# Kernel optimization log

Hardware: AMD Instinct MI355X
Metric: run time of the kernel (lower is better)

Reference implementation:

```python
import jax, jax.numpy as jnp
import numpy as np

T = 262144
S_IN, A_IN, S_OUT, G_OUT, H = 64, 16, 32, 16, 32


def setup_inputs() -> dict:
    key = jax.random.key(0)
    ks = jax.random.split(key, 16)
    def lin_w(k, i, o):
        return (jax.random.normal(k, (i, o), jnp.float32) / np.sqrt(i)).astype(jnp.float32)
    return {
        's': jax.random.normal(ks[0], (1, T, S_IN), jnp.float32),
        'a': jax.random.uniform(ks[1], (1, T, A_IN), jnp.float32),  # BCE targets in [0,1]
        'u': jax.random.uniform(ks[2], (1, T, 1), jnp.float32),     # Bernoulli noise
        'W1': lin_w(ks[3], 2 * (S_IN + A_IN), H), 'b1': jnp.zeros((H,), jnp.float32),
        'W2': lin_w(ks[4], 2 * H, H),             'b2': jnp.zeros((H,), jnp.float32),
        'W3': lin_w(ks[5], 2 * H, S_OUT + G_OUT + 1), 'b3': jnp.zeros((S_OUT + G_OUT + 1,), jnp.float32),
        'Wp1': lin_w(ks[6], S_IN + G_OUT, H),     'bp1': jnp.zeros((H,), jnp.float32),
        'Wp2': lin_w(ks[7], H, A_IN),             'bp2': jnp.zeros((A_IN,), jnp.float32),
    }


def gnn_layer(x, W, b):
    # GraphNetLayer: each node sees its own feature + global mean over the trajectory
    agg = jnp.broadcast_to(jnp.mean(x, axis=1, keepdims=True), x.shape)
    return jnp.concatenate([x, agg], axis=-1) @ W + b


def reference(s, a, u, W1, b1, W2, b2, W3, b3, Wp1, bp1, Wp2, bp2):
    # encode: GNN over [N,T,s_in+a_in]
    x = jnp.concatenate([s, a], axis=-1)
    h = jnp.tanh(gnn_layer(x, W1, b1))
    h = jnp.tanh(gnn_layer(h, W2, b2))
    out = gnn_layer(h, W3, b3)
    z, g, alpha_logit = jnp.split(out, [S_OUT, S_OUT + G_OUT], axis=-1)
    alpha = jax.nn.sigmoid(alpha_logit)

    # Bernoulli sample with externalized noise; no gradient through the sample
    hard_alpha = jax.lax.stop_gradient((u < alpha).astype(alpha.dtype))  # [1,T,1]
    log_probs = hard_alpha * jax.nn.log_sigmoid(alpha_logit) + (1.0 - hard_alpha) * jax.nn.log_sigmoid(-alpha_logit)
    reinforce_lp = jnp.mean(log_probs)

    # extend_goals_hard: carry last goal where alpha fired (N==1), ragged scan
    def step(prev, ga):
        gt, at = ga  # [G_OUT], [1]
        cur = jnp.where(at > 0, gt, prev)
        return cur, cur
    _, hard_g = jax.lax.scan(step, jnp.zeros((G_OUT,), g.dtype), (g[0], hard_alpha[0]))
    hard_g = hard_g[None]  # [1,T,G_OUT]

    # decode: goal-conditioned policy MLP
    logits = jnp.tanh(jnp.concatenate([s, hard_g], axis=-1) @ Wp1 + bp1) @ Wp2 + bp2

    # BCEWithLogits recon loss (use_prior=False, train_dynamics/correspondence=False)
    recon = -(a * jax.nn.log_sigmoid(logits) + (1.0 - a) * jax.nn.log_sigmoid(-logits))
    per_ts = recon
    loss = jnp.mean(per_ts) + reinforce_lp * jnp.mean(jax.lax.stop_gradient(per_ts))

    # padded equivalents of short_z/short_g (ragged gather z[0,mask]) returned as masked tensors
    return loss, logits, hard_alpha, hard_g
```

## Files before the change

kernel.cpp:

```cpp
#include <hip/hip_runtime.h>
#include <math.h>


#define TT 262144
#define NBT 1024
#define NBR 512

__device__ __forceinline__ float spf32(float x) {
  return fmaxf(x, 0.f) + log1pf(expf(-fabsf(x)));
}

__device__ __forceinline__ double exp64(double x) {
  const double LOG2E  = 1.4426950408889634074;
  const double LN2_HI = 6.93147180369123816490e-01;
  const double LN2_LO = 1.90821492927058770002e-10;
  double kd = rint(x * LOG2E);
  double r  = fma(-kd, LN2_HI, x);
  r = fma(-kd, LN2_LO, r);
  double p = 2.08767569878681e-9;
  p = fma(p, r, 2.505210838544172e-8);
  p = fma(p, r, 2.755731922398589e-7);
  p = fma(p, r, 2.7557319223985893e-6);
  p = fma(p, r, 2.48015873015873e-5);
  p = fma(p, r, 1.984126984126984e-4);
  p = fma(p, r, 1.388888888888889e-3);
  p = fma(p, r, 8.333333333333333e-3);
  p = fma(p, r, 4.1666666666666664e-2);
  p = fma(p, r, 1.6666666666666666e-1);
  p = fma(p, r, 0.5);
  p = fma(p, r, 1.0);
  p = fma(p, r, 1.0);
  int k = (int)kd;
  long long sb = ((long long)(k + 1023)) << 52;
  return p * __longlong_as_double(sb);
}

__device__ __forceinline__ double tanh64(double x) {
  double ax = fmin(fabs(x), 19.0);
  double e = exp64(2.0 * ax);
  double t = 1.0 - 2.0 / (e + 1.0);
  return x >= 0.0 ? t : -t;
}

template <int C>
__global__ __launch_bounds__(256) void reduce_cols(const float* __restrict__ in,
                                                   double* __restrict__ part) {
  const int rpb = 256 / C;
  int col = threadIdx.x & (C - 1);
  int sub = threadIdx.x / C;
  long row0 = (long)blockIdx.x * rpb + sub;
  long stride = (long)NBR * rpb;
  double acc = 0.0;
  for (long r = row0; r < TT; r += stride) acc += (double)in[r * C + col];
  __shared__ double sm[256];
  sm[threadIdx.x] = acc;
  __syncthreads();
  if (threadIdx.x < C) {
    double s = 0.0;
#pragma unroll
    for (int i = 0; i < rpb; ++i) s += sm[i * C + threadIdx.x];
    part[(long)blockIdx.x * C + threadIdx.x] = s;
  }
}

__global__ __launch_bounds__(640) void prep1(const double* __restrict__ ps_s,
                                             const double* __restrict__ ps_a,
                                             const float* __restrict__ W1,
                                             const float* __restrict__ b1,
                                             double invT, double* __restrict__ c1) {
  __shared__ double partial[80][8];
  __shared__ double mx[80];
  int tid = threadIdx.x;
  int col = tid >> 3, sub = tid & 7;
  double ssum = 0.0;
  if (col < 64) {
#pragma unroll
    for (int i = 0; i < 64; ++i) ssum += ps_s[(sub * 64 + i) * 64 + col];
  } else {
    int c = col - 64;
#pragma unroll
    for (int i = 0; i < 64; ++i) ssum += ps_a[(sub * 64 + i) * 16 + c];
  }
  partial[col][sub] = ssum;
  __syncthreads();
  if (tid < 80) {
    double s = 0.0;
#pragma unroll
    for (int i = 0; i < 8; ++i) s += partial[tid][i];
    mx[tid] = s * invT;
  }
  __syncthreads();
  if (tid < 32) {
    double acc = (double)b1[tid];
    for (int j = 0; j < 80; ++j) acc += mx[j] * (double)W1[(80 + j) * 32 + tid];
    c1[tid] = acc;
  }
}

__global__ __launch_bounds__(256) void prep2(const double* __restrict__ ps,
                                             const float* __restrict__ W2,
                                             const float* __restrict__ b2,
                                             double invT, double* __restrict__ c2) {
  __shared__ double partial[32][8];
  __shared__ double mh[32];
  int tid = threadIdx.x;
  int col = tid >> 3, sub = tid & 7;
  double ssum = 0.0;
#pragma unroll
  for (int i = 0; i < 128; ++i) ssum += ps[(sub * 128 + i) * 32 + col];
  partial[col][sub] = ssum;
  __syncthreads();
  if (tid < 32) {
    double s = 0.0;
#pragma unroll
    for (int i = 0; i < 8; ++i) s += partial[tid][i];
    mh[tid] = s * invT;
  }
  __syncthreads();
  if (tid < 32) {
    double acc = (double)b2[tid];
    for (int j = 0; j < 32; ++j) acc += mh[j] * (double)W2[(32 + j) * 32 + tid];
    c2[tid] = acc;
  }
}

__global__ __launch_bounds__(256) void prep3(const double* __restrict__ ps,
                                             const float* __restrict__ W3,
                                             const float* __restrict__ b3,
                                             double invT, double* __restrict__ c3) {
  __shared__ double partial[32][8];
  __shared__ double mh[32];
  int tid = threadIdx.x;
  int col = tid >> 3, sub = tid & 7;
  double ssum = 0.0;
#pragma unroll
  for (int i = 0; i < 128; ++i) ssum += ps[(sub * 128 + i) * 32 + col];
  partial[col][sub] = ssum;
  __syncthreads();
  if (tid < 32) {
    double s = 0.0;
#pragma unroll
    for (int i = 0; i < 8; ++i) s += partial[tid][i];
    mh[tid] = s * invT;
  }
  __syncthreads();
  if (tid < 17) {
    double acc = (double)b3[32 + tid];
    for (int j = 0; j < 32; ++j) acc += mh[j] * (double)W3[(32 + j) * 49 + 32 + tid];
    c3[tid] = acc;
  }
}


__global__ __launch_bounds__(256, 2) void h1_kernel(const float* __restrict__ s,
                                                    const float* __restrict__ a,
                                                    const float* __restrict__ W1,
                                                    const double* __restrict__ c1,
                                                    double* __restrict__ h,
                                                    double* __restrict__ ps_h) {
  __shared__ double Wl[80 * 32];
  __shared__ double ws[4 * 32];
  for (int i = threadIdx.x; i < 80 * 32; i += 256) Wl[i] = (double)W1[i];
  __syncthreads();
  long t = (long)blockIdx.x * 256 + threadIdx.x;
  double acc[32];
#pragma unroll
  for (int k = 0; k < 32; ++k) acc[k] = c1[k];
  const float4* s4 = (const float4*)(s + t * 64);
#pragma unroll 2
  for (int q = 0; q < 16; ++q) {
    float4 v = s4[q];
    const double* w = &Wl[(q * 4) * 32];
    double x0 = (double)v.x, x1 = (double)v.y, x2 = (double)v.z, x3 = (double)v.w;
#pragma unroll
    for (int k = 0; k < 32; ++k)
      acc[k] += x0 * w[k] + x1 * w[32 + k] + x2 * w[64 + k] + x3 * w[96 + k];
  }
  const float4* a4 = (const float4*)(a + t * 16);
#pragma unroll 2
  for (int q = 0; q < 4; ++q) {
    float4 v = a4[q];
    const double* w = &Wl[(64 + q * 4) * 32];
    double x0 = (double)v.x, x1 = (double)v.y, x2 = (double)v.z, x3 = (double)v.w;
#pragma unroll
    for (int k = 0; k < 32; ++k)
      acc[k] += x0 * w[k] + x1 * w[32 + k] + x2 * w[64 + k] + x3 * w[96 + k];
  }
  double* o = h + (size_t)blockIdx.x * 8192 + threadIdx.x;
#pragma unroll
  for (int k = 0; k < 32; ++k) { acc[k] = tanh64(acc[k]); o[k * 256] = acc[k]; }
  int lane = threadIdx.x & 63, wave = threadIdx.x >> 6;
#pragma unroll
  for (int k = 0; k < 32; ++k) {
    double v = acc[k];
    v += __shfl_down(v, 32, 64); v += __shfl_down(v, 16, 64);
    v += __shfl_down(v, 8, 64);  v += __shfl_down(v, 4, 64);
    v += __shfl_down(v, 2, 64);  v += __shfl_down(v, 1, 64);
    if (lane == 0) ws[wave * 32 + k] = v;
  }
  __syncthreads();
  if (threadIdx.x < 32) {
    double ssum = ws[threadIdx.x] + ws[32 + threadIdx.x] + ws[64 + threadIdx.x] +
                  ws[96 + threadIdx.x];
    ps_h[blockIdx.x * 32 + threadIdx.x] = ssum;
  }
}

__global__ __launch_bounds__(256, 2) void h2_kernel(const double* __restrict__ hin,
                                                    const float* __restrict__ W2,
                                                    const double* __restrict__ c2,
                                                    double* __restrict__ hout,
                                                    double* __restrict__ ps_h) {
  __shared__ double Wl[32 * 32];
  __shared__ double ws[4 * 32];
  for (int i = threadIdx.x; i < 32 * 32; i += 256) Wl[i] = (double)W2[i];
  __syncthreads();
  const double* x = hin + (size_t)blockIdx.x * 8192 + threadIdx.x;
  double acc[32];
#pragma unroll
  for (int k = 0; k < 32; ++k) acc[k] = c2[k];
#pragma unroll 4
  for (int j = 0; j < 32; ++j) {
    double xj = x[j * 256];
#pragma unroll
    for (int k = 0; k < 32; ++k) acc[k] += xj * Wl[j * 32 + k];
  }
  double* o = hout + (size_t)blockIdx.x * 8192 + threadIdx.x;
#pragma unroll
  for (int k = 0; k < 32; ++k) { acc[k] = tanh64(acc[k]); o[k * 256] = acc[k]; }
  int lane = threadIdx.x & 63, wave = threadIdx.x >> 6;
#pragma unroll
  for (int k = 0; k < 32; ++k) {
    double v = acc[k];
    v += __shfl_down(v, 32, 64); v += __shfl_down(v, 16, 64);
    v += __shfl_down(v, 8, 64);  v += __shfl_down(v, 4, 64);
    v += __shfl_down(v, 2, 64);  v += __shfl_down(v, 1, 64);
    if (lane == 0) ws[wave * 32 + k] = v;
  }
  __syncthreads();
  if (threadIdx.x < 32) {
    double ssum = ws[threadIdx.x] + ws[32 + threadIdx.x] + ws[64 + threadIdx.x] +
                  ws[96 + threadIdx.x];
    ps_h[blockIdx.x * 32 + threadIdx.x] = ssum;
  }
}

__global__ __launch_bounds__(256, 2) void out_kernel(const double* __restrict__ h,
                                                     const float* __restrict__ W3,
                                                     const double* __restrict__ c3,
                                                     const float* __restrict__ u,
                                                     float* __restrict__ g, float* __restrict__ ha,
                                                     int* __restrict__ lastf,
                                                     double* __restrict__ lp_part) {
  __shared__ double Wl[32 * 17];
  __shared__ double sm[256];
  __shared__ unsigned long long wm[4];
  for (int i = threadIdx.x; i < 32 * 17; i += 256) {
    int j = i / 17, k = i - j * 17;
    Wl[i] = (double)W3[j * 49 + 32 + k];
  }
  __syncthreads();
  long t = (long)blockIdx.x * 256 + threadIdx.x;
  const double* x = h + (size_t)blockIdx.x * 8192 + threadIdx.x;
  double acc[17];
#pragma unroll
  for (int k = 0; k < 17; ++k) acc[k] = c3[k];
#pragma unroll 4
  for (int j = 0; j < 32; ++j) {
    double xj = x[j * 256];
#pragma unroll
    for (int k = 0; k < 17; ++k) acc[k] += xj * Wl[j * 17 + k];
  }
  float4* g4 = (float4*)(g + t * 16);
  float4 o0, o1, o2, o3;
  o0.x = (float)acc[0];  o0.y = (float)acc[1];  o0.z = (float)acc[2];  o0.w = (float)acc[3];
  o1.x = (float)acc[4];  o1.y = (float)acc[5];  o1.z = (float)acc[6];  o1.w = (float)acc[7];
  o2.x = (float)acc[8];  o2.y = (float)acc[9];  o2.z = (float)acc[10]; o2.w = (float)acc[11];
  o3.x = (float)acc[12]; o3.y = (float)acc[13]; o3.z = (float)acc[14]; o3.w = (float)acc[15];
  g4[0] = o0; g4[1] = o1; g4[2] = o2; g4[3] = o3;
  double l = acc[16];
  double lc = fmin(fmax(l, -700.0), 700.0);
  double alpha = 1.0 / (1.0 + exp64(-lc));
  bool fired = ((double)u[t]) < alpha;
  ha[t] = fired ? 1.f : 0.f;
  float lf = (float)l;
  sm[threadIdx.x] = (double)(fired ? -spf32(-lf) : -spf32(lf));
  unsigned long long bm = __ballot(fired ? 1 : 0);
  if ((threadIdx.x & 63) == 0) wm[threadIdx.x >> 6] = bm;
  __syncthreads();
  for (int off = 128; off > 0; off >>= 1) {
    if (threadIdx.x < off) sm[threadIdx.x] += sm[threadIdx.x + off];
    __syncthreads();
  }
  if (threadIdx.x == 0) {
    lp_part[blockIdx.x] = sm[0];
    int last = -1;
#pragma unroll
    for (int w = 3; w >= 0; --w) {
      if (last < 0 && wm[w])
        last = (int)((long)blockIdx.x * 256 + w * 64 + (63 - __builtin_clzll(wm[w])));
    }
    lastf[blockIdx.x] = last;
  }
}

__global__ __launch_bounds__(1024) void carry_scan(const int* __restrict__ lastf,
                                                   int* __restrict__ carry, int n) {
  __shared__ int sm[1024];
  int tid = threadIdx.x;
  sm[tid] = (tid < n) ? lastf[tid] : -1;
  __syncthreads();
  for (int off = 1; off < n; off <<= 1) {
    int v = sm[tid];
    int o = (tid >= off) ? sm[tid - off] : -1;
    __syncthreads();
    sm[tid] = v > o ? v : o;
    __syncthreads();
  }
  if (tid < n) carry[tid] = (tid == 0) ? -1 : sm[tid - 1];
}

__global__ __launch_bounds__(256, 2) void decode_kernel(
    const float* __restrict__ s, const float* __restrict__ a, const float* __restrict__ g,
    const float* __restrict__ Wp1, const float* __restrict__ bp1, const float* __restrict__ Wp2,
    const float* __restrict__ bp2, const float* __restrict__ ha, const int* __restrict__ carry,
    float* __restrict__ logits, float* __restrict__ hardg, double* __restrict__ rc_part) {
  __shared__ float W1l[80 * 32];
  __shared__ float W2l[32 * 16];
  __shared__ int wlast[4];
  __shared__ double sm[256];
  long t = (long)blockIdx.x * 256 + threadIdx.x;
  bool fired = ha[t] > 0.5f;
  unsigned long long m = __ballot(fired ? 1 : 0);
  int wave = threadIdx.x >> 6, lane = threadIdx.x & 63;
  if (lane == 0)
    wlast[wave] = m ? (int)((long)blockIdx.x * 256 + wave * 64 + (63 - __builtin_clzll(m))) : -1;
  for (int i = threadIdx.x; i < 80 * 32; i += 256) W1l[i] = Wp1[i];
  for (int i = threadIdx.x; i < 32 * 16; i += 256) W2l[i] = Wp2[i];
  __syncthreads();
  unsigned long long pm = m & (~0ULL >> (63 - lane));
  int idx = pm ? (int)((long)blockIdx.x * 256 + wave * 64 + (63 - __builtin_clzll(pm))) : -1;
#pragma unroll
  for (int w = 0; w < 4; ++w)
    if (w < wave && wlast[w] > idx) idx = wlast[w];
  int cr = carry[blockIdx.x];
  if (cr > idx) idx = cr;
  float msk = idx >= 0 ? 1.f : 0.f;
  const float4* g4 = (const float4*)(g + (long)(idx >= 0 ? idx : 0) * 16);
  float4 v0 = g4[0], v1 = g4[1], v2 = g4[2], v3 = g4[3];
  float hg0  = msk * v0.x, hg1  = msk * v0.y, hg2  = msk * v0.z, hg3  = msk * v0.w;
  float hg4  = msk * v1.x, hg5  = msk * v1.y, hg6  = msk * v1.z, hg7  = msk * v1.w;
  float hg8  = msk * v2.x, hg9  = msk * v2.y, hg10 = msk * v2.z, hg11 = msk * v2.w;
  float hg12 = msk * v3.x, hg13 = msk * v3.y, hg14 = msk * v3.z, hg15 = msk * v3.w;
  hardg[t * 16 + 0]  = hg0;  hardg[t * 16 + 1]  = hg1;
  hardg[t * 16 + 2]  = hg2;  hardg[t * 16 + 3]  = hg3;
  hardg[t * 16 + 4]  = hg4;  hardg[t * 16 + 5]  = hg5;
  hardg[t * 16 + 6]  = hg6;  hardg[t * 16 + 7]  = hg7;
  hardg[t * 16 + 8]  = hg8;  hardg[t * 16 + 9]  = hg9;
  hardg[t * 16 + 10] = hg10; hardg[t * 16 + 11] = hg11;
  hardg[t * 16 + 12] = hg12; hardg[t * 16 + 13] = hg13;
  hardg[t * 16 + 14] = hg14; hardg[t * 16 + 15] = hg15;
  float acc[32];
#pragma unroll
  for (int k = 0; k < 32; ++k) {
    float v = bp1[k];
    v += hg0  * W1l[(64 + 0)  * 32 + k];  v += hg1  * W1l[(64 + 1)  * 32 + k];
    v += hg2  * W1l[(64 + 2)  * 32 + k];  v += hg3  * W1l[(64 + 3)  * 32 + k];
    v += hg4  * W1l[(64 + 4)  * 32 + k];  v += hg5  * W1l[(64 + 5)  * 32 + k];
    v += hg6  * W1l[(64 + 6)  * 32 + k];  v += hg7  * W1l[(64 + 7)  * 32 + k];
    v += hg8  * W1l[(64 + 8)  * 32 + k];  v += hg9  * W1l[(64 + 9)  * 32 + k];
    v += hg10 * W1l[(64 + 10) * 32 + k];  v += hg11 * W1l[(64 + 11) * 32 + k];
    v += hg12 * W1l[(64 + 12) * 32 + k];  v += hg13 * W1l[(64 + 13) * 32 + k];
    v += hg14 * W1l[(64 + 14) * 32 + k];  v += hg15 * W1l[(64 + 15) * 32 + k];
    acc[k] = v;
  }
  const float4* s4 = (const float4*)(s + t * 64);
#pragma unroll 4
  for (int q = 0; q < 16; ++q) {
    float4 v = s4[q];
    const float* w = &W1l[(q * 4) * 32];
#pragma unroll
    for (int k = 0; k < 32; ++k)
      acc[k] += v.x * w[k] + v.y * w[32 + k] + v.z * w[64 + k] + v.w * w[96 + k];
  }
#pragma unroll
  for (int k = 0; k < 32; ++k) acc[k] = tanhf(acc[k]);
  float lg[16];
#pragma unroll
  for (int k = 0; k < 16; ++k) lg[k] = bp2[k];
#pragma unroll
  for (int j = 0; j < 32; ++j) {
    float hj = acc[j];
    const float* w = &W2l[j * 16];
#pragma unroll
    for (int k = 0; k < 16; ++k) lg[k] += hj * w[k];
  }
#pragma unroll
  for (int k = 0; k < 16; ++k) logits[t * 16 + k] = lg[k];
  const float4* a4 = (const float4*)(a + t * 16);
  double rs = 0.0;
#pragma unroll
  for (int q = 0; q < 4; ++q) {
    float4 av = a4[q];
    float l0 = lg[q * 4], l1 = lg[q * 4 + 1], l2 = lg[q * 4 + 2], l3 = lg[q * 4 + 3];
    rs += (double)(av.x * spf32(-l0) + (1.f - av.x) * spf32(l0));
    rs += (double)(av.y * spf32(-l1) + (1.f - av.y) * spf32(l1));
    rs += (double)(av.z * spf32(-l2) + (1.f - av.z) * spf32(l2));
    rs += (double)(av.w * spf32(-l3) + (1.f - av.w) * spf32(l3));
  }
  sm[threadIdx.x] = rs;
  __syncthreads();
  for (int off = 128; off > 0; off >>= 1) {
    if (threadIdx.x < off) sm[threadIdx.x] += sm[threadIdx.x + off];
    __syncthreads();
  }
  if (threadIdx.x == 0) rc_part[blockIdx.x] = sm[0];
}

__global__ __launch_bounds__(256) void finalize(const double* __restrict__ lp_part,
                                                const double* __restrict__ rc_part, int nb,
                                                double invT, float* __restrict__ out0) {
  __shared__ double s1[256], s2[256];
  int tid = threadIdx.x;
  double a1 = 0, a2 = 0;
  for (int i = tid; i < nb; i += 256) { a1 += lp_part[i]; a2 += rc_part[i]; }
  s1[tid] = a1; s2[tid] = a2;
  __syncthreads();
  for (int off = 128; off > 0; off >>= 1) {
    if (tid < off) { s1[tid] += s1[tid + off]; s2[tid] += s2[tid + off]; }
    __syncthreads();
  }
  if (tid == 0) {
    double R = s1[0] * invT;
    double M = s2[0] * invT / 16.0;
    out0[0] = (float)(M + R * M);
  }
}

extern "C" void kernel_launch(void* const* d_in, const int* in_sizes, int n_in,
                              void* d_out, int out_size, void* d_ws, size_t ws_size,
                              hipStream_t stream) {
  const float* s   = (const float*)d_in[0];
  const float* a   = (const float*)d_in[1];
  const float* u   = (const float*)d_in[2];
  const float* W1  = (const float*)d_in[3];
  const float* b1  = (const float*)d_in[4];
  const float* W2  = (const float*)d_in[5];
  const float* b2  = (const float*)d_in[6];
  const float* W3  = (const float*)d_in[7];
  const float* b3  = (const float*)d_in[8];
  const float* Wp1 = (const float*)d_in[9];
  const float* bp1 = (const float*)d_in[10];
  const float* Wp2 = (const float*)d_in[11];
  const float* bp2 = (const float*)d_in[12];

  const double invT = 1.0 / (double)TT;

  double* h      = (double*)d_ws;
  double* ps_s   = h + (size_t)TT * 32;
  double* ps_a   = ps_s + (size_t)NBR * 64;
  double* ps_h   = ps_a + (size_t)NBR * 16;
  double* c1     = ps_h + (size_t)NBT * 32;
  double* c2     = c1 + 32;
  double* c3     = c2 + 32;
  double* lp_part= c3 + 24;
  double* rc_part= lp_part + NBT;
  float*  g      = (float*)(rc_part + NBT);
  int*    lastf  = (int*)(g + (size_t)TT * 16);
  int*    carry  = lastf + NBT;

  float* out    = (float*)d_out;
  float* loss   = out;
  float* logits = out + 1;
  float* ha     = out + 1 + (size_t)TT * 16;
  float* hg     = ha + TT;

  reduce_cols<64><<<NBR, 256, 0, stream>>>(s, ps_s);
  reduce_cols<16><<<NBR, 256, 0, stream>>>(a, ps_a);
  prep1<<<1, 640, 0, stream>>>(ps_s, ps_a, W1, b1, invT, c1);
  h1_kernel<<<NBT, 256, 0, stream>>>(s, a, W1, c1, h, ps_h);
  prep2<<<1, 256, 0, stream>>>(ps_h, W2, b2, invT, c2);
  h2_kernel<<<NBT, 256, 0, stream>>>(h, W2, c2, h, ps_h);
  prep3<<<1, 256, 0, stream>>>(ps_h, W3, b3, invT, c3);
  out_kernel<<<NBT, 256, 0, stream>>>(h, W3, c3, u, g, ha, lastf, lp_part);
  carry_scan<<<1, NBT, 0, stream>>>(lastf, carry, NBT);
  decode_kernel<<<NBT, 256, 0, stream>>>(s, a, g, Wp1, bp1, Wp2, bp2, ha, carry,
                                         logits, hg, rc_part);
  finalize<<<1, 256, 0, stream>>>(lp_part, rc_part, NBT, invT, loss);
}
```

Baseline: 321.2 us.

## Fuse all stages into one persistent kernel with hierarchical grid barriers

Replaces the eleven separate kernel launches with a single persistent kernel of 512 blocks, each handling two 256-row tiles. Stages are separated by a software grid barrier that uses atomic counters split across eight slots and a spin-wait flag, with one block doing the serial reduction steps between barriers. The goal is to remove launch overhead and the idle gaps caused by the single-block prep and scan kernels. In exchange it depends on all 512 blocks being co-resident, adds spin-wait latency at every barrier, and needs an extra memset each call.

```diff
diff --git a/kernel.cpp b/kernel.cpp
--- a/kernel.cpp
+++ b/kernel.cpp
@@ -3,8 +3,9 @@
 
 
 #define TT 262144
-#define NBT 1024
-#define NBR 512
+#define NTILE 1024
+#define NBLK 512
+#define INVT (1.0 / 262144.0)
 
 __device__ __forceinline__ float spf32(float x) {
   return fmaxf(x, 0.f) + log1pf(expf(-fabsf(x)));
@@ -42,398 +43,425 @@
   return x >= 0.0 ? t : -t;
 }
 
-template <int C>
-__global__ __launch_bounds__(256) void reduce_cols(const float* __restrict__ in,
-                                                   double* __restrict__ part) {
-  const int rpb = 256 / C;
-  int col = threadIdx.x & (C - 1);
-  int sub = threadIdx.x / C;
-  long row0 = (long)blockIdx.x * rpb + sub;
-  long stride = (long)NBR * rpb;
-  double acc = 0.0;
-  for (long r = row0; r < TT; r += stride) acc += (double)in[r * C + col];
-  __shared__ double sm[256];
-  sm[threadIdx.x] = acc;
+union ShMem {
+  struct { double Wl[80 * 32]; double ws[4 * 32]; } p2;
+  struct { double Wl[32 * 32]; double ws[4 * 32]; } p4;
+  struct { double Wl[32 * 17]; double sm[256]; unsigned long long wm[4]; } p6;
+  struct { double tmp[256]; double m[96]; } red;
+  struct { double sm[256]; } p0;
+  struct { int sc[1024]; } p7;
+  struct { float W1l[80 * 32]; float W2l[32 * 16]; double sm[256]; int wlast[4]; } p8;
+  struct { double s1[256]; double s2[256]; } p9;
+};
+
+__device__ __forceinline__ void gbar(unsigned* bar, int slot) {
   __syncthreads();
-  if (threadIdx.x < C) {
-    double s = 0.0;
-#pragma unroll
-    for (int i = 0; i < rpb; ++i) s += sm[i * C + threadIdx.x];
-    part[(long)blockIdx.x * C + threadIdx.x] = s;
-  }
+  if (threadIdx.x == 0) {
+    __threadfence();
+    unsigned* b = bar + slot * 16;
+    unsigned old = atomicAdd(&b[blockIdx.x & 7], 1u);
+    if (old == (NBLK / 8) - 1) {
+      unsigned t2 = atomicAdd(&b[8], 1u);
+      if (t2 == 7)
+        __hip_atomic_store(&b[9], 1u, __ATOMIC_RELAXED, __HIP_MEMORY_SCOPE_AGENT);
+    }
+    while (__hip_atomic_load(&b[9], __ATOMIC_RELAXED, __HIP_MEMORY_SCOPE_AGENT) == 0u)
+      __builtin_amdgcn_s_sleep(1);
+    __threadfence();
+  }
+  __syncthreads();
 }
 
-__global__ __launch_bounds__(640) void prep1(const double* __restrict__ ps_s,
-                                             const double* __restrict__ ps_a,
-                                             const float* __restrict__ W1,
-                                             const float* __restrict__ b1,
-                                             double invT, double* __restrict__ c1) {
-  __shared__ double partial[80][8];
-  __shared__ double mx[80];
-  int tid = threadIdx.x;
-  int col = tid >> 3, sub = tid & 7;
-  double ssum = 0.0;
-  if (col < 64) {
-#pragma unroll
-    for (int i = 0; i < 64; ++i) ssum += ps_s[(sub * 64 + i) * 64 + col];
-  } else {
-    int c = col - 64;
-#pragma unroll
-    for (int i = 0; i < 64; ++i) ssum += ps_a[(sub * 64 + i) * 16 + c];
-  }
-  partial[col][sub] = ssum;
-  __syncthreads();
-  if (tid < 80) {
-    double s = 0.0;
-#pragma unroll
-    for (int i = 0; i < 8; ++i) s += partial[tid][i];
-    mx[tid] = s * invT;
-  }
-  __syncthreads();
-  if (tid < 32) {
-    double acc = (double)b1[tid];
-    for (int j = 0; j < 80; ++j) acc += mx[j] * (double)W1[(80 + j) * 32 + tid];
-    c1[tid] = acc;
-  }
-}
-
-__global__ __launch_bounds__(256) void prep2(const double* __restrict__ ps,
-                                             const float* __restrict__ W2,
-                                             const float* __restrict__ b2,
-                                             double invT, double* __restrict__ c2) {
-  __shared__ double partial[32][8];
-  __shared__ double mh[32];
-  int tid = threadIdx.x;
-  int col = tid >> 3, sub = tid & 7;
-  double ssum = 0.0;
-#pragma unroll
-  for (int i = 0; i < 128; ++i) ssum += ps[(sub * 128 + i) * 32 + col];
-  partial[col][sub] = ssum;
-  __syncthreads();
-  if (tid < 32) {
-    double s = 0.0;
-#pragma unroll
-    for (int i = 0; i < 8; ++i) s += partial[tid][i];
-    mh[tid] = s * invT;
-  }
-  __syncthreads();
-  if (tid < 32) {
-    double acc = (double)b2[tid];
-    for (int j = 0; j < 32; ++j) acc += mh[j] * (double)W2[(32 + j) * 32 + tid];
-    c2[tid] = acc;
-  }
-}
-
-__global__ __launch_bounds__(256) void prep3(const double* __restrict__ ps,
-                                             const float* __restrict__ W3,
-                                             const float* __restrict__ b3,
-                                             double invT, double* __restrict__ c3) {
-  __shared__ double partial[32][8];
-  __shared__ double mh[32];
-  int tid = threadIdx.x;
-  int col = tid >> 3, sub = tid & 7;
-  double ssum = 0.0;
-#pragma unroll
-  for (int i = 0; i < 128; ++i) ssum += ps[(sub * 128 + i) * 32 + col];
-  partial[col][sub] = ssum;
-  __syncthreads();
-  if (tid < 32) {
-    double s = 0.0;
-#pragma unroll
-    for (int i = 0; i < 8; ++i) s += partial[tid][i];
-    mh[tid] = s * invT;
-  }
-  __syncthreads();
-  if (tid < 17) {
-    double acc = (double)b3[32 + tid];
-    for (int j = 0; j < 32; ++j) acc += mh[j] * (double)W3[(32 + j) * 49 + 32 + tid];
-    c3[tid] = acc;
-  }
-}
-
-
-__global__ __launch_bounds__(256, 2) void h1_kernel(const float* __restrict__ s,
-                                                    const float* __restrict__ a,
-                                                    const float* __restrict__ W1,
-                                                    const double* __restrict__ c1,
-                                                    double* __restrict__ h,
-                                                    double* __restrict__ ps_h) {
-  __shared__ double Wl[80 * 32];
-  __shared__ double ws[4 * 32];
-  for (int i = threadIdx.x; i < 80 * 32; i += 256) Wl[i] = (double)W1[i];
-  __syncthreads();
-  long t = (long)blockIdx.x * 256 + threadIdx.x;
-  double acc[32];
-#pragma unroll
-  for (int k = 0; k < 32; ++k) acc[k] = c1[k];
-  const float4* s4 = (const float4*)(s + t * 64);
+__global__ __launch_bounds__(256, 2) void mega(
+    const float* __restrict__ s, const float* __restrict__ a, const float* __restrict__ u,
+    const float* __restrict__ W1, const float* __restrict__ b1,
+    const float* __restrict__ W2, const float* __restrict__ b2,
+    const float* __restrict__ W3, const float* __restrict__ b3,
+    const float* __restrict__ Wp1, const float* __restrict__ bp1,
+    const float* __restrict__ Wp2, const float* __restrict__ bp2,
+    double* __restrict__ h, double* __restrict__ ps_s, double* __restrict__ ps_a,
+    double* __restrict__ ps_h,
+    double* __restrict__ c1v, double* __restrict__ c2v, double* __restrict__ c3v,
+    double* __restrict__ lp_part, double* __restrict__ rc_part,
+    float* __restrict__ g, int* __restrict__ lastf, int* __restrict__ carry,
+    float* __restrict__ loss, float* __restrict__ logits,
+    float* __restrict__ ha_out, float* __restrict__ hg_out, unsigned* bar)
+{
+  __shared__ ShMem sh;
+  const int tid = threadIdx.x;
+  const int bid = blockIdx.x;
+
+#pragma unroll 1
+  for (int tt = 0; tt < 2; ++tt) {
+    const int tb = bid + tt * NBLK;
+    const long base = (long)tb * 256;
+    int col = tid & 63, sub = tid >> 6;
+    double acc0 = 0.0;
+    for (int r = sub * 64; r < sub * 64 + 64; ++r)
+      acc0 += (double)s[(base + r) * 64 + col];
+    sh.p0.sm[tid] = acc0;
+    __syncthreads();
+    if (tid < 64)
+      ps_s[tb * 64 + tid] = sh.p0.sm[tid] + sh.p0.sm[64 + tid] +
+                            sh.p0.sm[128 + tid] + sh.p0.sm[192 + tid];
+    __syncthreads();
+    int colA = tid & 15, subA = tid >> 4;
+    double accA = 0.0;
+    for (int r = subA * 16; r < subA * 16 + 16; ++r)
+      accA += (double)a[(base + r) * 16 + colA];
+    sh.p0.sm[tid] = accA;
+    __syncthreads();
+    if (tid < 16) {
+      double sa = 0.0;
+#pragma unroll
+      for (int i = 0; i < 16; ++i) sa += sh.p0.sm[i * 16 + tid];
+      ps_a[tb * 16 + tid] = sa;
+    }
+    __syncthreads();
+  }
+  gbar(bar, 0);
+
+  if (bid == 0) {
+    int c = tid & 63, sub = tid >> 6;
+    double acc0 = 0.0;
+    for (int i = 0; i < 256; ++i) acc0 += ps_s[(sub * 256 + i) * 64 + c];
+    sh.red.tmp[tid] = acc0;
+    __syncthreads();
+    if (tid < 64)
+      sh.red.m[tid] = (sh.red.tmp[tid] + sh.red.tmp[64 + tid] +
+                       sh.red.tmp[128 + tid] + sh.red.tmp[192 + tid]) * INVT;
+    __syncthreads();
+    int cA = tid & 15, subA = tid >> 4;
+    double accA = 0.0;
+    for (int i = 0; i < 64; ++i) accA += ps_a[(subA * 64 + i) * 16 + cA];
+    sh.red.tmp[tid] = accA;
+    __syncthreads();
+    if (tid < 16) {
+      double sa = 0.0;
+#pragma unroll
+      for (int i = 0; i < 16; ++i) sa += sh.red.tmp[i * 16 + tid];
+      sh.red.m[64 + tid] = sa * INVT;
+    }
+    __syncthreads();
+    if (tid < 32) {
+      double acc = (double)b1[tid];
+      for (int j = 0; j < 80; ++j) acc += sh.red.m[j] * (double)W1[(80 + j) * 32 + tid];
+      c1v[tid] = acc;
+    }
+  }
+  gbar(bar, 1);
+
+  {
+    for (int i = tid; i < 80 * 32; i += 256) sh.p2.Wl[i] = (double)W1[i];
+    __syncthreads();
+#pragma unroll 1
+    for (int tt = 0; tt < 2; ++tt) {
+      const int tb = bid + tt * NBLK;
+      const long t = (long)tb * 256 + tid;
+      double acc[32];
+#pragma unroll
+      for (int k = 0; k < 32; ++k) acc[k] = c1v[k];
+      const float4* s4 = (const float4*)(s + t * 64);
 #pragma unroll 2
-  for (int q = 0; q < 16; ++q) {
-    float4 v = s4[q];
-    const double* w = &Wl[(q * 4) * 32];
-    double x0 = (double)v.x, x1 = (double)v.y, x2 = (double)v.z, x3 = (double)v.w;
-#pragma unroll
-    for (int k = 0; k < 32; ++k)
-      acc[k] += x0 * w[k] + x1 * w[32 + k] + x2 * w[64 + k] + x3 * w[96 + k];
-  }
-  const float4* a4 = (const float4*)(a + t * 16);
+      for (int q = 0; q < 16; ++q) {
+        float4 v = s4[q];
+        const double* w = &sh.p2.Wl[(q * 4) * 32];
+        double x0 = (double)v.x, x1 = (double)v.y, x2 = (double)v.z, x3 = (double)v.w;
+#pragma unroll
+        for (int k = 0; k < 32; ++k)
+          acc[k] += x0 * w[k] + x1 * w[32 + k] + x2 * w[64 + k] + x3 * w[96 + k];
+      }
+      const float4* a4 = (const float4*)(a + t * 16);
 #pragma unroll 2
-  for (int q = 0; q < 4; ++q) {
-    float4 v = a4[q];
-    const double* w = &Wl[(64 + q * 4) * 32];
-    double x0 = (double)v.x, x1 = (double)v.y, x2 = (double)v.z, x3 = (double)v.w;
-#pragma unroll
-    for (int k = 0; k < 32; ++k)
-      acc[k] += x0 * w[k] + x1 * w[32 + k] + x2 * w[64 + k] + x3 * w[96 + k];
-  }
-  double* o = h + (size_t)blockIdx.x * 8192 + threadIdx.x;
-#pragma unroll
-  for (int k = 0; k < 32; ++k) { acc[k] = tanh64(acc[k]); o[k * 256] = acc[k]; }
-  int lane = threadIdx.x & 63, wave = threadIdx.x >> 6;
-#pragma unroll
-  for (int k = 0; k < 32; ++k) {
-    double v = acc[k];
-    v += __shfl_down(v, 32, 64); v += __shfl_down(v, 16, 64);
-    v += __shfl_down(v, 8, 64);  v += __shfl_down(v, 4, 64);
-    v += __shfl_down(v, 2, 64);  v += __shfl_down(v, 1, 64);
-    if (lane == 0) ws[wave * 32 + k] = v;
-  }
-  __syncthreads();
-  if (threadIdx.x < 32) {
-    double ssum = ws[threadIdx.x] + ws[32 + threadIdx.x] + ws[64 + threadIdx.x] +
-                  ws[96 + threadIdx.x];
-    ps_h[blockIdx.x * 32 + threadIdx.x] = ssum;
-  }
-}
-
-__global__ __launch_bounds__(256, 2) void h2_kernel(const double* __restrict__ hin,
-                                                    const float* __restrict__ W2,
-                                                    const double* __restrict__ c2,
-                                                    double* __restrict__ hout,
-                                                    double* __restrict__ ps_h) {
-  __shared__ double Wl[32 * 32];
-  __shared__ double ws[4 * 32];
-  for (int i = threadIdx.x; i < 32 * 32; i += 256) Wl[i] = (double)W2[i];
-  __syncthreads();
-  const double* x = hin + (size_t)blockIdx.x * 8192 + threadIdx.x;
-  double acc[32];
-#pragma unroll
-  for (int k = 0; k < 32; ++k) acc[k] = c2[k];
+      for (int q = 0; q < 4; ++q) {
+        float4 v = a4[q];
+        const double* w = &sh.p2.Wl[(64 + q * 4) * 32];
+        double x0 = (double)v.x, x1 = (double)v.y, x2 = (double)v.z, x3 = (double)v.w;
+#pragma unroll
+        for (int k = 0; k < 32; ++k)
+          acc[k] += x0 * w[k] + x1 * w[32 + k] + x2 * w[64 + k] + x3 * w[96 + k];
+      }
+      double* o = h + (size_t)tb * 8192 + tid;
+#pragma unroll
+      for (int k = 0; k < 32; ++k) { acc[k] = tanh64(acc[k]); o[k * 256] = acc[k]; }
+      int lane = tid & 63, wave = tid >> 6;
+#pragma unroll
+      for (int k = 0; k < 32; ++k) {
+        double v = acc[k];
+        v += __shfl_down(v, 32, 64); v += __shfl_down(v, 16, 64);
+        v += __shfl_down(v, 8, 64);  v += __shfl_down(v, 4, 64);
+        v += __shfl_down(v, 2, 64);  v += __shfl_down(v, 1, 64);
+        if (lane == 0) sh.p2.ws[wave * 32 + k] = v;
+      }
+      __syncthreads();
+      if (tid < 32)
+        ps_h[tb * 32 + tid] = sh.p2.ws[tid] + sh.p2.ws[32 + tid] +
+                              sh.p2.ws[64 + tid] + sh.p2.ws[96 + tid];
+      __syncthreads();
+    }
+  }
+  gbar(bar, 2);
+
+  if (bid == 0) {
+    int c = tid & 31, sub = tid >> 5;
+    double acc0 = 0.0;
+    for (int i = 0; i < 128; ++i) acc0 += ps_h[(sub * 128 + i) * 32 + c];
+    sh.red.tmp[tid] = acc0;
+    __syncthreads();
+    if (tid < 32) {
+      double sa = 0.0;
+#pragma unroll
+      for (int i = 0; i < 8; ++i) sa += sh.red.tmp[i * 32 + tid];
+      sh.red.m[tid] = sa * INVT;
+    }
+    __syncthreads();
+    if (tid < 32) {
+      double acc = (double)b2[tid];
+      for (int j = 0; j < 32; ++j) acc += sh.red.m[j] * (double)W2[(32 + j) * 32 + tid];
+      c2v[tid] = acc;
+    }
+  }
+  gbar(bar, 3);
+
+  {
+    for (int i = tid; i < 32 * 32; i += 256) sh.p4.Wl[i] = (double)W2[i];
+    __syncthreads();
+#pragma unroll 1
+    for (int tt = 0; tt < 2; ++tt) {
+      const int tb = bid + tt * NBLK;
+      const double* x = h + (size_t)tb * 8192 + tid;
+      double acc[32];
+#pragma unroll
+      for (int k = 0; k < 32; ++k) acc[k] = c2v[k];
 #pragma unroll 4
-  for (int j = 0; j < 32; ++j) {
-    double xj = x[j * 256];
-#pragma unroll
-    for (int k = 0; k < 32; ++k) acc[k] += xj * Wl[j * 32 + k];
-  }
-  double* o = hout + (size_t)blockIdx.x * 8192 + threadIdx.x;
-#pragma unroll
-  for (int k = 0; k < 32; ++k) { acc[k] = tanh64(acc[k]); o[k * 256] = acc[k]; }
-  int lane = threadIdx.x & 63, wave = threadIdx.x >> 6;
-#pragma unroll
-  for (int k = 0; k < 32; ++k) {
-    double v = acc[k];
-    v += __shfl_down(v, 32, 64); v += __shfl_down(v, 16, 64);
-    v += __shfl_down(v, 8, 64);  v += __shfl_down(v, 4, 64);
-    v += __shfl_down(v, 2, 64);  v += __shfl_down(v, 1, 64);
-    if (lane == 0) ws[wave * 32 + k] = v;
-  }
-  __syncthreads();
-  if (threadIdx.x < 32) {
-    double ssum = ws[threadIdx.x] + ws[32 + threadIdx.x] + ws[64 + threadIdx.x] +
-                  ws[96 + threadIdx.x];
-    ps_h[blockIdx.x * 32 + threadIdx.x] = ssum;
-  }
-}
-
-__global__ __launch_bounds__(256, 2) void out_kernel(const double* __restrict__ h,
-                                                     const float* __restrict__ W3,
-                                                     const double* __restrict__ c3,
-                                                     const float* __restrict__ u,
-                                                     float* __restrict__ g, float* __restrict__ ha,
-                                                     int* __restrict__ lastf,
-                                                     double* __restrict__ lp_part) {
-  __shared__ double Wl[32 * 17];
-  __shared__ double sm[256];
-  __shared__ unsigned long long wm[4];
-  for (int i = threadIdx.x; i < 32 * 17; i += 256) {
-    int j = i / 17, k = i - j * 17;
-    Wl[i] = (double)W3[j * 49 + 32 + k];
-  }
-  __syncthreads();
-  long t = (long)blockIdx.x * 256 + threadIdx.x;
-  const double* x = h + (size_t)blockIdx.x * 8192 + threadIdx.x;
-  double acc[17];
-#pragma unroll
-  for (int k = 0; k < 17; ++k) acc[k] = c3[k];
+      for (int j = 0; j < 32; ++j) {
+        double xj = x[j * 256];
+#pragma unroll
+        for (int k = 0; k < 32; ++k) acc[k] += xj * sh.p4.Wl[j * 32 + k];
+      }
+      double* o = h + (size_t)tb * 8192 + tid;
+#pragma unroll
+      for (int k = 0; k < 32; ++k) { acc[k] = tanh64(acc[k]); o[k * 256] = acc[k]; }
+      int lane = tid & 63, wave = tid >> 6;
+#pragma unroll
+      for (int k = 0; k < 32; ++k) {
+        double v = acc[k];
+        v += __shfl_down(v, 32, 64); v += __shfl_down(v, 16, 64);
+        v += __shfl_down(v, 8, 64);  v += __shfl_down(v, 4, 64);
+        v += __shfl_down(v, 2, 64);  v += __shfl_down(v, 1, 64);
+        if (lane == 0) sh.p4.ws[wave * 32 + k] = v;
+      }
+      __syncthreads();
+      if (tid < 32)
+        ps_h[tb * 32 + tid] = sh.p4.ws[tid] + sh.p4.ws[32 + tid] +
+                              sh.p4.ws[64 + tid] + sh.p4.ws[96 + tid];
+      __syncthreads();
+    }
+  }
+  gbar(bar, 4);
+
+  if (bid == 0) {
+    int c = tid & 31, sub = tid >> 5;
+    double acc0 = 0.0;
+    for (int i = 0; i < 128; ++i) acc0 += ps_h[(sub * 128 + i) * 32 + c];
+    sh.red.tmp[tid] = acc0;
+    __syncthreads();
+    if (tid < 32) {
+      double sa = 0.0;
+#pragma unroll
+      for (int i = 0; i < 8; ++i) sa += sh.red.tmp[i * 32 + tid];
+      sh.red.m[tid] = sa * INVT;
+    }
+    __syncthreads();
+    if (tid < 17) {
+      double acc = (double)b3[32 + tid];
+      for (int j = 0; j < 32; ++j) acc += sh.red.m[j] * (double)W3[(32 + j) * 49 + 32 + tid];
+      c3v[tid] = acc;
+    }
+  }
+  gbar(bar, 5);
+
+  {
+    for (int i = tid; i < 32 * 17; i += 256) {
+      int j = i / 17, k = i - j * 17;
+      sh.p6.Wl[i] = (double)W3[j * 49 + 32 + k];
+    }
+    __syncthreads();
+#pragma unroll 1
+    for (int tt = 0; tt < 2; ++tt) {
+      const int tb = bid + tt * NBLK;
+      const long t = (long)tb * 256 + tid;
+      const double* x = h + (size_t)tb * 8192 + tid;
+      double acc[17];
+#pragma unroll
+      for (int k = 0; k < 17; ++k) acc[k] = c3v[k];
 #pragma unroll 4
-  for (int j = 0; j < 32; ++j) {
-    double xj = x[j * 256];
-#pragma unroll
-    for (int k = 0; k < 17; ++k) acc[k] += xj * Wl[j * 17 + k];
-  }
-  float4* g4 = (float4*)(g + t * 16);
-  float4 o0, o1, o2, o3;
-  o0.x = (float)acc[0];  o0.y = (float)acc[1];  o0.z = (float)acc[2];  o0.w = (float)acc[3];
-  o1.x = (float)acc[4];  o1.y = (float)acc[5];  o1.z = (float)acc[6];  o1.w = (float)acc[7];
-  o2.x = (float)acc[8];  o2.y = (float)acc[9];  o2.z = (float)acc[10]; o2.w = (float)acc[11];
-  o3.x = (float)acc[12]; o3.y = (float)acc[13]; o3.z = (float)acc[14]; o3.w = (float)acc[15];
-  g4[0] = o0; g4[1] = o1; g4[2] = o2; g4[3] = o3;
-  double l = acc[16];
-  double lc = fmin(fmax(l, -700.0), 700.0);
-  double alpha = 1.0 / (1.0 + exp64(-lc));
-  bool fired = ((double)u[t]) < alpha;
-  ha[t] = fired ? 1.f : 0.f;
-  float lf = (float)l;
-  sm[threadIdx.x] = (double)(fired ? -spf32(-lf) : -spf32(lf));
-  unsigned long long bm = __ballot(fired ? 1 : 0);
-  if ((threadIdx.x & 63) == 0) wm[threadIdx.x >> 6] = bm;
-  __syncthreads();
-  for (int off = 128; off > 0; off >>= 1) {
-    if (threadIdx.x < off) sm[threadIdx.x] += sm[threadIdx.x + off];
-    __syncthreads();
-  }
-  if (threadIdx.x == 0) {
-    lp_part[blockIdx.x] = sm[0];
-    int last = -1;
-#pragma unroll
-    for (int w = 3; w >= 0; --w) {
-      if (last < 0 && wm[w])
-        last = (int)((long)blockIdx.x * 256 + w * 64 + (63 - __builtin_clzll(wm[w])));
-    }
-    lastf[blockIdx.x] = last;
-  }
-}
-
-__global__ __launch_bounds__(1024) void carry_scan(const int* __restrict__ lastf,
-                                                   int* __restrict__ carry, int n) {
-  __shared__ int sm[1024];
-  int tid = threadIdx.x;
-  sm[tid] = (tid < n) ? lastf[tid] : -1;
-  __syncthreads();
-  for (int off = 1; off < n; off <<= 1) {
-    int v = sm[tid];
-    int o = (tid >= off) ? sm[tid - off] : -1;
-    __syncthreads();
-    sm[tid] = v > o ? v : o;
-    __syncthreads();
-  }
-  if (tid < n) carry[tid] = (tid == 0) ? -1 : sm[tid - 1];
-}
-
-__global__ __launch_bounds__(256, 2) void decode_kernel(
-    const float* __restrict__ s, const float* __restrict__ a, const float* __restrict__ g,
-    const float* __restrict__ Wp1, const float* __restrict__ bp1, const float* __restrict__ Wp2,
-    const float* __restrict__ bp2, const float* __restrict__ ha, const int* __restrict__ carry,
-    float* __restrict__ logits, float* __restrict__ hardg, double* __restrict__ rc_part) {
-  __shared__ float W1l[80 * 32];
-  __shared__ float W2l[32 * 16];
-  __shared__ int wlast[4];
-  __shared__ double sm[256];
-  long t = (long)blockIdx.x * 256 + threadIdx.x;
-  bool fired = ha[t] > 0.5f;
-  unsigned long long m = __ballot(fired ? 1 : 0);
-  int wave = threadIdx.x >> 6, lane = threadIdx.x & 63;
-  if (lane == 0)
-    wlast[wave] = m ? (int)((long)blockIdx.x * 256 + wave * 64 + (63 - __builtin_clzll(m))) : -1;
-  for (int i = threadIdx.x; i < 80 * 32; i += 256) W1l[i] = Wp1[i];
-  for (int i = threadIdx.x; i < 32 * 16; i += 256) W2l[i] = Wp2[i];
-  __syncthreads();
-  unsigned long long pm = m & (~0ULL >> (63 - lane));
-  int idx = pm ? (int)((long)blockIdx.x * 256 + wave * 64 + (63 - __builtin_clzll(pm))) : -1;
-#pragma unroll
-  for (int w = 0; w < 4; ++w)
-    if (w < wave && wlast[w] > idx) idx = wlast[w];
-  int cr = carry[blockIdx.x];
-  if (cr > idx) idx = cr;
-  float msk = idx >= 0 ? 1.f : 0.f;
-  const float4* g4 = (const float4*)(g + (long)(idx >= 0 ? idx : 0) * 16);
-  float4 v0 = g4[0], v1 = g4[1], v2 = g4[2], v3 = g4[3];
-  float hg0  = msk * v0.x, hg1  = msk * v0.y, hg2  = msk * v0.z, hg3  = msk * v0.w;
-  float hg4  = msk * v1.x, hg5  = msk * v1.y, hg6  = msk * v1.z, hg7  = msk * v1.w;
-  float hg8  = msk * v2.x, hg9  = msk * v2.y, hg10 = msk * v2.z, hg11 = msk * v2.w;
-  float hg12 = msk * v3.x, hg13 = msk * v3.y, hg14 = msk * v3.z, hg15 = msk * v3.w;
-  hardg[t * 16 + 0]  = hg0;  hardg[t * 16 + 1]  = hg1;
-  hardg[t * 16 + 2]  = hg2;  hardg[t * 16 + 3]  = hg3;
-  hardg[t * 16 + 4]  = hg4;  hardg[t * 16 + 5]  = hg5;
-  hardg[t * 16 + 6]  = hg6;  hardg[t * 16 + 7]  = hg7;
-  hardg[t * 16 + 8]  = hg8;  hardg[t * 16 + 9]  = hg9;
-  hardg[t * 16 + 10] = hg10; hardg[t * 16 + 11] = hg11;
-  hardg[t * 16 + 12] = hg12; hardg[t * 16 + 13] = hg13;
-  hardg[t * 16 + 14] = hg14; hardg[t * 16 + 15] = hg15;
-  float acc[32];
-#pragma unroll
-  for (int k = 0; k < 32; ++k) {
-    float v = bp1[k];
-    v += hg0  * W1l[(64 + 0)  * 32 + k];  v += hg1  * W1l[(64 + 1)  * 32 + k];
-    v += hg2  * W1l[(64 + 2)  * 32 + k];  v += hg3  * W1l[(64 + 3)  * 32 + k];
-    v += hg4  * W1l[(64 + 4)  * 32 + k];  v += hg5  * W1l[(64 + 5)  * 32 + k];
-    v += hg6  * W1l[(64 + 6)  * 32 + k];  v += hg7  * W1l[(64 + 7)  * 32 + k];
-    v += hg8  * W1l[(64 + 8)  * 32 + k];  v += hg9  * W1l[(64 + 9)  * 32 + k];
-    v += hg10 * W1l[(64 + 10) * 32 + k];  v += hg11 * W1l[(64 + 11) * 32 + k];
-    v += hg12 * W1l[(64 + 12) * 32 + k];  v += hg13 * W1l[(64 + 13) * 32 + k];
-    v += hg14 * W1l[(64 + 14) * 32 + k];  v += hg15 * W1l[(64 + 15) * 32 + k];
-    acc[k] = v;
-  }
-  const float4* s4 = (const float4*)(s + t * 64);
+      for (int j = 0; j < 32; ++j) {
+        double xj = x[j * 256];
+#pragma unroll
+        for (int k = 0; k < 17; ++k) acc[k] += xj * sh.p6.Wl[j * 17 + k];
+      }
+      float4* g4 = (float4*)(g + t * 16);
+      float4 o0, o1, o2, o3;
+      o0.x = (float)acc[0];  o0.y = (float)acc[1];  o0.z = (float)acc[2];  o0.w = (float)acc[3];
+      o1.x = (float)acc[4];  o1.y = (float)acc[5];  o1.z = (float)acc[6];  o1.w = (float)acc[7];
+      o2.x = (float)acc[8];  o2.y = (float)acc[9];  o2.z = (float)acc[10]; o2.w = (float)acc[11];
+      o3.x = (float)acc[12]; o3.y = (float)acc[13]; o3.z = (float)acc[14]; o3.w = (float)acc[15];
+      g4[0] = o0; g4[1] = o1; g4[2] = o2; g4[3] = o3;
+      double l = acc[16];
+      double lc = fmin(fmax(l, -700.0), 700.0);
+      double alpha = 1.0 / (1.0 + exp64(-lc));
+      bool fired = ((double)u[t]) < alpha;
+      ha_out[t] = fired ? 1.f : 0.f;
+      float lf = (float)l;
+      sh.p6.sm[tid] = (double)(fired ? -spf32(-lf) : -spf32(lf));
+      unsigned long long bm = __ballot(fired ? 1 : 0);
+      if ((tid & 63) == 0) sh.p6.wm[tid >> 6] = bm;
+      __syncthreads();
+      for (int off = 128; off > 0; off >>= 1) {
+        if (tid < off) sh.p6.sm[tid] += sh.p6.sm[tid + off];
+        __syncthreads();
+      }
+      if (tid == 0) {
+        lp_part[tb] = sh.p6.sm[0];
+        int last = -1;
+#pragma unroll
+        for (int w = 3; w >= 0; --w)
+          if (last < 0 && sh.p6.wm[w])
+            last = (int)((long)tb * 256 + w * 64 + (63 - __builtin_clzll(sh.p6.wm[w])));
+        lastf[tb] = last;
+      }
+      __syncthreads();
+    }
+  }
+  gbar(bar, 6);
+
+  if (bid == 0) {
+    for (int i = tid; i < 1024; i += 256) sh.p7.sc[i] = lastf[i];
+    __syncthreads();
+    for (int off = 1; off < 1024; off <<= 1) {
+      int i0 = tid, i1 = tid + 256, i2 = tid + 512, i3 = tid + 768;
+      int v0 = (i0 >= off && sh.p7.sc[i0 - off] > sh.p7.sc[i0]) ? sh.p7.sc[i0 - off] : sh.p7.sc[i0];
+      int v1 = (i1 >= off && sh.p7.sc[i1 - off] > sh.p7.sc[i1]) ? sh.p7.sc[i1 - off] : sh.p7.sc[i1];
+      int v2 = (i2 >= off && sh.p7.sc[i2 - off] > sh.p7.sc[i2]) ? sh.p7.sc[i2 - off] : sh.p7.sc[i2];
+      int v3 = (i3 >= off && sh.p7.sc[i3 - off] > sh.p7.sc[i3]) ? sh.p7.sc[i3 - off] : sh.p7.sc[i3];
+      __syncthreads();
+      sh.p7.sc[i0] = v0; sh.p7.sc[i1] = v1; sh.p7.sc[i2] = v2; sh.p7.sc[i3] = v3;
+      __syncthreads();
+    }
+    for (int i = tid; i < 1024; i += 256) carry[i] = (i == 0) ? -1 : sh.p7.sc[i - 1];
+  }
+  gbar(bar, 7);
+
+  {
+    for (int i = tid; i < 80 * 32; i += 256) sh.p8.W1l[i] = Wp1[i];
+    for (int i = tid; i < 32 * 16; i += 256) sh.p8.W2l[i] = Wp2[i];
+#pragma unroll 1
+    for (int tt = 0; tt < 2; ++tt) {
+      const int tb = bid + tt * NBLK;
+      const long t = (long)tb * 256 + tid;
+      bool fired = ha_out[t] > 0.5f;
+      unsigned long long m = __ballot(fired ? 1 : 0);
+      int wave = tid >> 6, lane = tid & 63;
+      if (lane == 0)
+        sh.p8.wlast[wave] = m ? (int)((long)tb * 256 + wave * 64 + (63 - __builtin_clzll(m))) : -1;
+      __syncthreads();
+      unsigned long long pm = m & (~0ULL >> (63 - lane));
+      int idx = pm ? (int)((long)tb * 256 + wave * 64 + (63 - __builtin_clzll(pm))) : -1;
+#pragma unroll
+      for (int w = 0; w < 4; ++w)
+        if (w < wave && sh.p8.wlast[w] > idx) idx = sh.p8.wlast[w];
+      int cr = carry[tb];
+      if (cr > idx) idx = cr;
+      float msk = idx >= 0 ? 1.f : 0.f;
+      const float4* g4 = (const float4*)(g + (long)(idx >= 0 ? idx : 0) * 16);
+      float4 v0 = g4[0], v1 = g4[1], v2 = g4[2], v3 = g4[3];
+      float hg0  = msk * v0.x, hg1  = msk * v0.y, hg2  = msk * v0.z, hg3  = msk * v0.w;
+      float hg4  = msk * v1.x, hg5  = msk * v1.y, hg6  = msk * v1.z, hg7  = msk * v1.w;
+      float hg8  = msk * v2.x, hg9  = msk * v2.y, hg10 = msk * v2.z, hg11 = msk * v2.w;
+      float hg12 = msk * v3.x, hg13 = msk * v3.y, hg14 = msk * v3.z, hg15 = msk * v3.w;
+      hg_out[t * 16 + 0]  = hg0;  hg_out[t * 16 + 1]  = hg1;
+      hg_out[t * 16 + 2]  = hg2;  hg_out[t * 16 + 3]  = hg3;
+      hg_out[t * 16 + 4]  = hg4;  hg_out[t * 16 + 5]  = hg5;
+      hg_out[t * 16 + 6]  = hg6;  hg_out[t * 16 + 7]  = hg7;
+      hg_out[t * 16 + 8]  = hg8;  hg_out[t * 16 + 9]  = hg9;
+      hg_out[t * 16 + 10] = hg10; hg_out[t * 16 + 11] = hg11;
+      hg_out[t * 16 + 12] = hg12; hg_out[t * 16 + 13] = hg13;
+      hg_out[t * 16 + 14] = hg14; hg_out[t * 16 + 15] = hg15;
+      float acc[32];
+#pragma unroll
+      for (int k = 0; k < 32; ++k) {
+        float v = bp1[k];
+        v += hg0  * sh.p8.W1l[(64 + 0)  * 32 + k];  v += hg1  * sh.p8.W1l[(64 + 1)  * 32 + k];
+        v += hg2  * sh.p8.W1l[(64 + 2)  * 32 + k];  v += hg3  * sh.p8.W1l[(64 + 3)  * 32 + k];
+        v += hg4  * sh.p8.W1l[(64 + 4)  * 32 + k];  v += hg5  * sh.p8.W1l[(64 + 5)  * 32 + k];
+        v += hg6  * sh.p8.W1l[(64 + 6)  * 32 + k];  v += hg7  * sh.p8.W1l[(64 + 7)  * 32 + k];
+        v += hg8  * sh.p8.W1l[(64 + 8)  * 32 + k];  v += hg9  * sh.p8.W1l[(64 + 9)  * 32 + k];
+        v += hg10 * sh.p8.W1l[(64 + 10) * 32 + k];  v += hg11 * sh.p8.W1l[(64 + 11) * 32 + k];
+        v += hg12 * sh.p8.W1l[(64 + 12) * 32 + k];  v += hg13 * sh.p8.W1l[(64 + 13) * 32 + k];
+        v += hg14 * sh.p8.W1l[(64 + 14) * 32 + k];  v += hg15 * sh.p8.W1l[(64 + 15) * 32 + k];
+        acc[k] = v;
+      }
+      const float4* s4 = (const float4*)(s + t * 64);
 #pragma unroll 4
-  for (int q = 0; q < 16; ++q) {
-    float4 v = s4[q];
-    const float* w = &W1l[(q * 4) * 32];
-#pragma unroll
-    for (int k = 0; k < 32; ++k)
-      acc[k] += v.x * w[k] + v.y * w[32 + k] + v.z * w[64 + k] + v.w * w[96 + k];
-  }
-#pragma unroll
-  for (int k = 0; k < 32; ++k) acc[k] = tanhf(acc[k]);
-  float lg[16];
-#pragma unroll
-  for (int k = 0; k < 16; ++k) lg[k] = bp2[k];
-#pragma unroll
-  for (int j = 0; j < 32; ++j) {
-    float hj = acc[j];
-    const float* w = &W2l[j * 16];
-#pragma unroll
-    for (int k = 0; k < 16; ++k) lg[k] += hj * w[k];
-  }
-#pragma unroll
-  for (int k = 0; k < 16; ++k) logits[t * 16 + k] = lg[k];
-  const float4* a4 = (const float4*)(a + t * 16);
-  double rs = 0.0;
-#pragma unroll
-  for (int q = 0; q < 4; ++q) {
-    float4 av = a4[q];
-    float l0 = lg[q * 4], l1 = lg[q * 4 + 1], l2 = lg[q * 4 + 2], l3 = lg[q * 4 + 3];
-    rs += (double)(av.x * spf32(-l0) + (1.f - av.x) * spf32(l0));
-    rs += (double)(av.y * spf32(-l1) + (1.f - av.y) * spf32(l1));
-    rs += (double)(av.z * spf32(-l2) + (1.f - av.z) * spf32(l2));
-    rs += (double)(av.w * spf32(-l3) + (1.f - av.w) * spf32(l3));
-  }
-  sm[threadIdx.x] = rs;
-  __syncthreads();
-  for (int off = 128; off > 0; off >>= 1) {
-    if (threadIdx.x < off) sm[threadIdx.x] += sm[threadIdx.x + off];
-    __syncthreads();
-  }
-  if (threadIdx.x == 0) rc_part[blockIdx.x] = sm[0];
-}
-
-__global__ __launch_bounds__(256) void finalize(const double* __restrict__ lp_part,
-                                                const double* __restrict__ rc_part, int nb,
-                                                double invT, float* __restrict__ out0) {
-  __shared__ double s1[256], s2[256];
-  int tid = threadIdx.x;
-  double a1 = 0, a2 = 0;
-  for (int i = tid; i < nb; i += 256) { a1 += lp_part[i]; a2 += rc_part[i]; }
-  s1[tid] = a1; s2[tid] = a2;
-  __syncthreads();
-  for (int off = 128; off > 0; off >>= 1) {
-    if (tid < off) { s1[tid] += s1[tid + off]; s2[tid] += s2[tid + off]; }
-    __syncthreads();
-  }
-  if (tid == 0) {
-    double R = s1[0] * invT;
-    double M = s2[0] * invT / 16.0;
-    out0[0] = (float)(M + R * M);
+      for (int q = 0; q < 16; ++q) {
+        float4 v = s4[q];
+        const float* w = &sh.p8.W1l[(q * 4) * 32];
+#pragma unroll
+        for (int k = 0; k < 32; ++k)
+          acc[k] += v.x * w[k] + v.y * w[32 + k] + v.z * w[64 + k] + v.w * w[96 + k];
+      }
+#pragma unroll
+      for (int k = 0; k < 32; ++k) acc[k] = tanhf(acc[k]);
+      float lg[16];
+#pragma unroll
+      for (int k = 0; k < 16; ++k) lg[k] = bp2[k];
+#pragma unroll
+      for (int j = 0; j < 32; ++j) {
+        float hj = acc[j];
+        const float* w = &sh.p8.W2l[j * 16];
+#pragma unroll
+        for (int k = 0; k < 16; ++k) lg[k] += hj * w[k];
+      }
+#pragma unroll
+      for (int k = 0; k < 16; ++k) logits[t * 16 + k] = lg[k];
+      const float4* a4 = (const float4*)(a + t * 16);
+      double rs = 0.0;
+#pragma unroll
+      for (int q = 0; q < 4; ++q) {
+        float4 av = a4[q];
+        float l0 = lg[q * 4], l1 = lg[q * 4 + 1], l2 = lg[q * 4 + 2], l3 = lg[q * 4 + 3];
+        rs += (double)(av.x * spf32(-l0) + (1.f - av.x) * spf32(l0));
+        rs += (double)(av.y * spf32(-l1) + (1.f - av.y) * spf32(l1));
+        rs += (double)(av.z * spf32(-l2) + (1.f - av.z) * spf32(l2));
+        rs += (double)(av.w * spf32(-l3) + (1.f - av.w) * spf32(l3));
+      }
+      sh.p8.sm[tid] = rs;
+      __syncthreads();
+      for (int off = 128; off > 0; off >>= 1) {
+        if (tid < off) sh.p8.sm[tid] += sh.p8.sm[tid + off];
+        __syncthreads();
+      }
+      if (tid == 0) rc_part[tb] = sh.p8.sm[0];
+      __syncthreads();
+    }
+  }
+  gbar(bar, 8);
+
+  if (bid == 0) {
+    double a1 = 0.0, a2 = 0.0;
+    for (int i = tid; i < 1024; i += 256) { a1 += lp_part[i]; a2 += rc_part[i]; }
+    sh.p9.s1[tid] = a1; sh.p9.s2[tid] = a2;
+    __syncthreads();
+    for (int off = 128; off > 0; off >>= 1) {
+      if (tid < off) { sh.p9.s1[tid] += sh.p9.s1[tid + off]; sh.p9.s2[tid] += sh.p9.s2[tid + off]; }
+      __syncthreads();
+    }
+    if (tid == 0) {
+      double R = sh.p9.s1[0] * INVT;
+      double M = sh.p9.s2[0] * INVT / 16.0;
+      loss[0] = (float)(M + R * M);
+    }
   }
 }
 
@@ -454,20 +482,19 @@
   const float* Wp2 = (const float*)d_in[11];
   const float* bp2 = (const float*)d_in[12];
 
-  const double invT = 1.0 / (double)TT;
-
   double* h      = (double*)d_ws;
   double* ps_s   = h + (size_t)TT * 32;
-  double* ps_a   = ps_s + (size_t)NBR * 64;
-  double* ps_h   = ps_a + (size_t)NBR * 16;
-  double* c1     = ps_h + (size_t)NBT * 32;
-  double* c2     = c1 + 32;
-  double* c3     = c2 + 32;
-  double* lp_part= c3 + 24;
-  double* rc_part= lp_part + NBT;
-  float*  g      = (float*)(rc_part + NBT);
+  double* ps_a   = ps_s + (size_t)NTILE * 64;
+  double* ps_h   = ps_a + (size_t)NTILE * 16;
+  double* c1v    = ps_h + (size_t)NTILE * 32;
+  double* c2v    = c1v + 32;
+  double* c3v    = c2v + 32;
+  double* lp     = c3v + 24;
+  double* rc     = lp + NTILE;
+  float*  g      = (float*)(rc + NTILE);
   int*    lastf  = (int*)(g + (size_t)TT * 16);
-  int*    carry  = lastf + NBT;
+  int*    carry  = lastf + NTILE;
+  unsigned* bar  = (unsigned*)(carry + NTILE);
 
   float* out    = (float*)d_out;
   float* loss   = out;
@@ -475,16 +502,9 @@
   float* ha     = out + 1 + (size_t)TT * 16;
   float* hg     = ha + TT;
 
-  reduce_cols<64><<<NBR, 256, 0, stream>>>(s, ps_s);
-  reduce_cols<16><<<NBR, 256, 0, stream>>>(a, ps_a);
-  prep1<<<1, 640, 0, stream>>>(ps_s, ps_a, W1, b1, invT, c1);
-  h1_kernel<<<NBT, 256, 0, stream>>>(s, a, W1, c1, h, ps_h);
-  prep2<<<1, 256, 0, stream>>>(ps_h, W2, b2, invT, c2);
-  h2_kernel<<<NBT, 256, 0, stream>>>(h, W2, c2, h, ps_h);
-  prep3<<<1, 256, 0, stream>>>(ps_h, W3, b3, invT, c3);
-  out_kernel<<<NBT, 256, 0, stream>>>(h, W3, c3, u, g, ha, lastf, lp_part);
-  carry_scan<<<1, NBT, 0, stream>>>(lastf, carry, NBT);
-  decode_kernel<<<NBT, 256, 0, stream>>>(s, a, g, Wp1, bp1, Wp2, bp2, ha, carry,
-                                         logits, hg, rc_part);
-  finalize<<<1, 256, 0, stream>>>(lp_part, rc_part, NBT, invT, loss);
+  hipMemsetAsync((void*)bar, 0, 9 * 16 * sizeof(unsigned), stream);
+  mega<<<dim3(NBLK), dim3(256), 0, stream>>>(
+      s, a, u, W1, b1, W2, b2, W3, b3, Wp1, bp1, Wp2, bp2,
+      h, ps_s, ps_a, ps_h, c1v, c2v, c3v, lp, rc,
+      g, lastf, carry, loss, logits, ha, hg, bar);
 }
```

After: 636.1 us. 1.98x slower.
